# Performance work log

Measured on AMD Instinct MI355X. Metric: run time of the kernel, lower is better.

Reference implementation:

```python
import jax, jax.numpy as jnp
import numpy as np
import math

B, H, S, D = 2, 16, 2048, 64


def setup_inputs() -> dict:
    key = jax.random.key(0)
    kq, kk, kv = jax.random.split(key, 3)
    q = jax.random.normal(kq, (B, H, S, D), dtype=jnp.float32)
    k = jax.random.normal(kk, (B, H, S, D), dtype=jnp.float32)
    v = jax.random.normal(kv, (B, H, S, D), dtype=jnp.float32)
    # causal lower-triangular mask, broadcastable to [B, H, S, S]
    mask = jnp.tril(jnp.ones((S, S), dtype=jnp.int32))[None, None, :, :]
    return {"q": q, "k": k, "v": v, "mask": mask}


def reference(q, k, v, mask):
    d_tensor = q.shape[-1]
    # scores: [B, H, S, S] = q @ k^T / sqrt(d)
    scores = jnp.einsum("bhqd,bhkd->bhqk", q, k) / math.sqrt(d_tensor)
    scores = jnp.where(mask == 0, jnp.float32(-100000.0), scores)
    attn = jax.nn.softmax(scores, axis=-1)
    out = jnp.einsum("bhqk,bhkd->bhqd", attn, v)
    return (out, attn)
```

## Files before the change

kernel.cpp:

```cpp
#include <hip/hip_runtime.h>

#define S_LEN 2048
#define D_DIM 64
#define NBH   32
#define BQ    64
#define SCALE2 0.1803368801f
#define KST   72
#define PST   76

typedef _Float16 half8 __attribute__((ext_vector_type(8)));
typedef _Float16 half4 __attribute__((ext_vector_type(4)));
typedef float    fx4   __attribute__((ext_vector_type(4)));

__global__ __launch_bounds__(256, 3)
void attn_fused(const float* __restrict__ Q, const float* __restrict__ K,
                const float* __restrict__ V, float* __restrict__ Out,
                float* __restrict__ Attn) {
    const int bh  = blockIdx.x;
    const int qt  = (int)(gridDim.y - 1) - (int)blockIdx.y;
    const int q0  = qt * BQ;
    const int T   = qt + 1;

    const int tid  = threadIdx.x;
    const int lane = tid & 63;
    const int w    = tid >> 6;
    const int ln15 = lane & 15;
    const int quad = lane >> 4;

    __shared__ _Float16 q_s[BQ][KST];
    __shared__ _Float16 k_s[64][KST];
    __shared__ _Float16 v_t[64][KST];
    __shared__ _Float16 p_s[4][16][PST];

    const float* Qb = Q + ((size_t)bh * S_LEN + q0) * D_DIM;
    const float* Kb = K + (size_t)bh * S_LEN * D_DIM;
    const float* Vb = V + (size_t)bh * S_LEN * D_DIM;

    {
        const float4* src = (const float4*)Qb;
        #pragma unroll
        for (int u = 0; u < 4; ++u) {
            int i = u * 256 + tid;
            int r = i >> 4, c4 = i & 15;
            float4 f = src[i];
            half4 h = {(_Float16)(f.x * SCALE2), (_Float16)(f.y * SCALE2),
                       (_Float16)(f.z * SCALE2), (_Float16)(f.w * SCALE2)};
            *(half4*)&q_s[r][c4 * 4] = h;
        }
    }
    __syncthreads();

    const int mrow = w * 16 + ln15;
    const half8 a_q0 = *(const half8*)&q_s[mrow][quad * 8];
    const half8 a_q1 = *(const half8*)&q_s[mrow][32 + quad * 8];

    const int qrow0 = q0 + w * 16 + quad * 4;

    const int sr  = tid >> 4;
    const int sc4 = tid & 15;

    float l_r[4] = {0.f, 0.f, 0.f, 0.f};

    float4 kf0, kf1, kf2, kf3;
    {
        const float4* ks = (const float4*)Kb;
        kf0 = ks[tid]; kf1 = ks[256 + tid]; kf2 = ks[512 + tid]; kf3 = ks[768 + tid];
    }
    for (int t = 0; t < T; ++t) {
        {
            half4 h0 = {(_Float16)kf0.x, (_Float16)kf0.y, (_Float16)kf0.z, (_Float16)kf0.w};
            half4 h1 = {(_Float16)kf1.x, (_Float16)kf1.y, (_Float16)kf1.z, (_Float16)kf1.w};
            half4 h2 = {(_Float16)kf2.x, (_Float16)kf2.y, (_Float16)kf2.z, (_Float16)kf2.w};
            half4 h3 = {(_Float16)kf3.x, (_Float16)kf3.y, (_Float16)kf3.z, (_Float16)kf3.w};
            *(half4*)&k_s[sr +  0][sc4 * 4] = h0;
            *(half4*)&k_s[sr + 16][sc4 * 4] = h1;
            *(half4*)&k_s[sr + 32][sc4 * 4] = h2;
            *(half4*)&k_s[sr + 48][sc4 * 4] = h3;
        }
        __syncthreads();

        if (t + 1 < T) {
            const float4* kn = (const float4*)(Kb + (size_t)(t + 1) * 64 * D_DIM);
            kf0 = kn[tid]; kf1 = kn[256 + tid]; kf2 = kn[512 + tid]; kf3 = kn[768 + tid];
        }

        fx4 sC[4];
        #pragma unroll
        for (int nt = 0; nt < 4; ++nt) {
            fx4 z = {0.f, 0.f, 0.f, 0.f};
            half8 b0 = *(const half8*)&k_s[nt * 16 + ln15][quad * 8];
            half8 b1 = *(const half8*)&k_s[nt * 16 + ln15][32 + quad * 8];
            z = __builtin_amdgcn_mfma_f32_16x16x32_f16(a_q0, b0, z, 0, 0, 0);
            z = __builtin_amdgcn_mfma_f32_16x16x32_f16(a_q1, b1, z, 0, 0, 0);
            sC[nt] = z;
        }

        if (t < T - 1) {
            #pragma unroll
            for (int nt = 0; nt < 4; ++nt)
                #pragma unroll
                for (int r = 0; r < 4; ++r)
                    l_r[r] += exp2f(sC[nt][r]);
        } else {
            const int j0 = t * 64;
            #pragma unroll
            for (int nt = 0; nt < 4; ++nt) {
                int jc = j0 + nt * 16 + ln15;
                #pragma unroll
                for (int r = 0; r < 4; ++r) {
                    float x = (jc <= qrow0 + r) ? sC[nt][r] : -1e30f;
                    l_r[r] += exp2f(x);
                }
            }
        }
        __syncthreads();
    }

    float inv_l[4];
    #pragma unroll
    for (int r = 0; r < 4; ++r) {
        float s = l_r[r];
        s += __shfl_xor(s, 1);
        s += __shfl_xor(s, 2);
        s += __shfl_xor(s, 4);
        s += __shfl_xor(s, 8);
        inv_l[r] = 1.0f / s;
    }

    fx4 oacc[4];
    #pragma unroll
    for (int dt = 0; dt < 4; ++dt) oacc[dt] = (fx4){0.f, 0.f, 0.f, 0.f};

    const int vc4 = tid >> 4;
    const int vjg = tid & 15;

    float4 vf0, vf1, vf2, vf3;
    {
        const float4* ks = (const float4*)Kb;
        kf0 = ks[tid]; kf1 = ks[256 + tid]; kf2 = ks[512 + tid]; kf3 = ks[768 + tid];
        const float4* vs = (const float4*)Vb;
        vf0 = vs[(vjg * 4 + 0) * 16 + vc4];
        vf1 = vs[(vjg * 4 + 1) * 16 + vc4];
        vf2 = vs[(vjg * 4 + 2) * 16 + vc4];
        vf3 = vs[(vjg * 4 + 3) * 16 + vc4];
    }

    for (int t = 0; t < T; ++t) {
        const int j0 = t * 64;

        {
            half4 h0 = {(_Float16)kf0.x, (_Float16)kf0.y, (_Float16)kf0.z, (_Float16)kf0.w};
            half4 h1 = {(_Float16)kf1.x, (_Float16)kf1.y, (_Float16)kf1.z, (_Float16)kf1.w};
            half4 h2 = {(_Float16)kf2.x, (_Float16)kf2.y, (_Float16)kf2.z, (_Float16)kf2.w};
            half4 h3 = {(_Float16)kf3.x, (_Float16)kf3.y, (_Float16)kf3.z, (_Float16)kf3.w};
            *(half4*)&k_s[sr +  0][sc4 * 4] = h0;
            *(half4*)&k_s[sr + 16][sc4 * 4] = h1;
            *(half4*)&k_s[sr + 32][sc4 * 4] = h2;
            *(half4*)&k_s[sr + 48][sc4 * 4] = h3;
            half4 t0 = {(_Float16)vf0.x, (_Float16)vf1.x, (_Float16)vf2.x, (_Float16)vf3.x};
            half4 t1 = {(_Float16)vf0.y, (_Float16)vf1.y, (_Float16)vf2.y, (_Float16)vf3.y};
            half4 t2 = {(_Float16)vf0.z, (_Float16)vf1.z, (_Float16)vf2.z, (_Float16)vf3.z};
            half4 t3 = {(_Float16)vf0.w, (_Float16)vf1.w, (_Float16)vf2.w, (_Float16)vf3.w};
            *(half4*)&v_t[vc4 * 4 + 0][vjg * 4] = t0;
            *(half4*)&v_t[vc4 * 4 + 1][vjg * 4] = t1;
            *(half4*)&v_t[vc4 * 4 + 2][vjg * 4] = t2;
            *(half4*)&v_t[vc4 * 4 + 3][vjg * 4] = t3;
        }
        __syncthreads();

        if (t + 1 < T) {
            const float4* kn = (const float4*)(Kb + (size_t)(t + 1) * 64 * D_DIM);
            kf0 = kn[tid]; kf1 = kn[256 + tid]; kf2 = kn[512 + tid]; kf3 = kn[768 + tid];
            const float4* vn = (const float4*)(Vb + (size_t)(t + 1) * 64 * D_DIM);
            vf0 = vn[(vjg * 4 + 0) * 16 + vc4];
            vf1 = vn[(vjg * 4 + 1) * 16 + vc4];
            vf2 = vn[(vjg * 4 + 2) * 16 + vc4];
            vf3 = vn[(vjg * 4 + 3) * 16 + vc4];
        }

        fx4 sC[4];
        #pragma unroll
        for (int nt = 0; nt < 4; ++nt) {
            fx4 z = {0.f, 0.f, 0.f, 0.f};
            half8 b0 = *(const half8*)&k_s[nt * 16 + ln15][quad * 8];
            half8 b1 = *(const half8*)&k_s[nt * 16 + ln15][32 + quad * 8];
            z = __builtin_amdgcn_mfma_f32_16x16x32_f16(a_q0, b0, z, 0, 0, 0);
            z = __builtin_amdgcn_mfma_f32_16x16x32_f16(a_q1, b1, z, 0, 0, 0);
            sC[nt] = z;
        }

        if (t < T - 1) {
            #pragma unroll
            for (int nt = 0; nt < 4; ++nt) {
                int jc = j0 + nt * 16 + ln15;
                #pragma unroll
                for (int r = 0; r < 4; ++r) {
                    float p = exp2f(sC[nt][r]) * inv_l[r];
                    Attn[((size_t)bh * S_LEN + (size_t)(qrow0 + r)) * S_LEN + jc] = p;
                    p_s[w][quad * 4 + r][nt * 16 + ln15] = (_Float16)p;
                }
            }
        } else {
            #pragma unroll
            for (int nt = 0; nt < 4; ++nt) {
                int jc = j0 + nt * 16 + ln15;
                #pragma unroll
                for (int r = 0; r < 4; ++r) {
                    float x = (jc <= qrow0 + r) ? sC[nt][r] : -1e30f;
                    float p = exp2f(x) * inv_l[r];
                    Attn[((size_t)bh * S_LEN + (size_t)(qrow0 + r)) * S_LEN + jc] = p;
                    p_s[w][quad * 4 + r][nt * 16 + ln15] = (_Float16)p;
                }
            }
        }

        {
            half8 a_p0 = *(const half8*)&p_s[w][ln15][quad * 8];
            half8 a_p1 = *(const half8*)&p_s[w][ln15][32 + quad * 8];
            #pragma unroll
            for (int dt = 0; dt < 4; ++dt) {
                half8 bv0 = *(const half8*)&v_t[dt * 16 + ln15][quad * 8];
                half8 bv1 = *(const half8*)&v_t[dt * 16 + ln15][32 + quad * 8];
                oacc[dt] = __builtin_amdgcn_mfma_f32_16x16x32_f16(a_p0, bv0, oacc[dt], 0, 0, 0);
                oacc[dt] = __builtin_amdgcn_mfma_f32_16x16x32_f16(a_p1, bv1, oacc[dt], 0, 0, 0);
            }
        }
        __syncthreads();
    }

    #pragma unroll
    for (int dt = 0; dt < 4; ++dt) {
        #pragma unroll
        for (int r = 0; r < 4; ++r) {
            size_t oidx = ((size_t)bh * S_LEN + (size_t)(qrow0 + r)) * D_DIM + dt * 16 + ln15;
            Out[oidx] = oacc[dt][r];
        }
    }

    {
        const int jend = q0 + BQ;
        const int rowlen4 = (S_LEN - jend) >> 2;
        if (rowlen4 > 0) {
            fx4 z = {0.f, 0.f, 0.f, 0.f};
            for (int r = w; r < BQ; r += 4) {
                fx4* dst = (fx4*)(Attn + ((size_t)bh * S_LEN + (size_t)(q0 + r)) * S_LEN + jend);
                for (int c = lane; c < rowlen4; c += 64) dst[c] = z;
            }
        }
    }
}

extern "C" void kernel_launch(void* const* d_in, const int* in_sizes, int n_in,
                              void* d_out, int out_size, void* d_ws, size_t ws_size,
                              hipStream_t stream) {
    const float* q = (const float*)d_in[0];
    const float* k = (const float*)d_in[1];
    const float* v = (const float*)d_in[2];
    float* out  = (float*)d_out;
    float* attn = out + (size_t)NBH * S_LEN * D_DIM;
    dim3 grid(NBH, S_LEN / BQ);
    attn_fused<<<grid, 256, 0, stream>>>(q, k, v, out, attn);
}
```

Baseline: 683.3 us.

## Double-buffer K/V tiles in LDS and use lighter barriers

```diff
diff --git a/kernel.cpp b/kernel.cpp
--- a/kernel.cpp
+++ b/kernel.cpp
@@ -6,11 +6,16 @@
 #define BQ    64
 #define SCALE2 0.1803368801f
 #define KST   72
-#define PST   76
 
 typedef _Float16 half8 __attribute__((ext_vector_type(8)));
 typedef _Float16 half4 __attribute__((ext_vector_type(4)));
 typedef float    fx4   __attribute__((ext_vector_type(4)));
+
+#define BAR() do {                                            \
+    asm volatile("s_waitcnt lgkmcnt(0)" ::: "memory");        \
+    __builtin_amdgcn_s_barrier();                             \
+    asm volatile("" ::: "memory");                            \
+} while (0)
 
 __global__ __launch_bounds__(256, 3)
 void attn_fused(const float* __restrict__ Q, const float* __restrict__ K,
@@ -27,15 +32,25 @@
     const int ln15 = lane & 15;
     const int quad = lane >> 4;
 
-    __shared__ _Float16 q_s[BQ][KST];
-    __shared__ _Float16 k_s[64][KST];
-    __shared__ _Float16 v_t[64][KST];
-    __shared__ _Float16 p_s[4][16][PST];
+    __shared__ _Float16 smem[5 * 64 * KST];
+    _Float16 (*kb0)[KST] = (_Float16 (*)[KST])&smem[0];
+    _Float16 (*kb1)[KST] = (_Float16 (*)[KST])&smem[64 * KST];
+    _Float16 (*vb0)[KST] = (_Float16 (*)[KST])&smem[2 * 64 * KST];
+    _Float16 (*vb1)[KST] = (_Float16 (*)[KST])&smem[3 * 64 * KST];
+    _Float16 (*pw)[KST]  = (_Float16 (*)[KST])&smem[4 * 64 * KST + w * 16 * KST];
+    _Float16 (*q_s)[KST] = kb1;
 
     const float* Qb = Q + ((size_t)bh * S_LEN + q0) * D_DIM;
     const float* Kb = K + (size_t)bh * S_LEN * D_DIM;
     const float* Vb = V + (size_t)bh * S_LEN * D_DIM;
 
+    const int sr  = tid >> 4;
+    const int sc4 = tid & 15;
+    const int vc4 = tid >> 4;
+    const int vjg = tid & 15;
+
+    const float4* ks0 = (const float4*)Kb;
+    float4 kf0 = ks0[tid], kf1 = ks0[256 + tid], kf2 = ks0[512 + tid], kf3 = ks0[768 + tid];
     {
         const float4* src = (const float4*)Qb;
         #pragma unroll
@@ -56,28 +71,21 @@
 
     const int qrow0 = q0 + w * 16 + quad * 4;
 
-    const int sr  = tid >> 4;
-    const int sc4 = tid & 15;
-
     float l_r[4] = {0.f, 0.f, 0.f, 0.f};
 
-    float4 kf0, kf1, kf2, kf3;
-    {
-        const float4* ks = (const float4*)Kb;
-        kf0 = ks[tid]; kf1 = ks[256 + tid]; kf2 = ks[512 + tid]; kf3 = ks[768 + tid];
-    }
     for (int t = 0; t < T; ++t) {
+        _Float16 (*kb)[KST] = (t & 1) ? kb1 : kb0;
         {
             half4 h0 = {(_Float16)kf0.x, (_Float16)kf0.y, (_Float16)kf0.z, (_Float16)kf0.w};
             half4 h1 = {(_Float16)kf1.x, (_Float16)kf1.y, (_Float16)kf1.z, (_Float16)kf1.w};
             half4 h2 = {(_Float16)kf2.x, (_Float16)kf2.y, (_Float16)kf2.z, (_Float16)kf2.w};
             half4 h3 = {(_Float16)kf3.x, (_Float16)kf3.y, (_Float16)kf3.z, (_Float16)kf3.w};
-            *(half4*)&k_s[sr +  0][sc4 * 4] = h0;
-            *(half4*)&k_s[sr + 16][sc4 * 4] = h1;
-            *(half4*)&k_s[sr + 32][sc4 * 4] = h2;
-            *(half4*)&k_s[sr + 48][sc4 * 4] = h3;
-        }
-        __syncthreads();
+            *(half4*)&kb[sr +  0][sc4 * 4] = h0;
+            *(half4*)&kb[sr + 16][sc4 * 4] = h1;
+            *(half4*)&kb[sr + 32][sc4 * 4] = h2;
+            *(half4*)&kb[sr + 48][sc4 * 4] = h3;
+        }
+        BAR();
 
         if (t + 1 < T) {
             const float4* kn = (const float4*)(Kb + (size_t)(t + 1) * 64 * D_DIM);
@@ -88,8 +96,8 @@
         #pragma unroll
         for (int nt = 0; nt < 4; ++nt) {
             fx4 z = {0.f, 0.f, 0.f, 0.f};
-            half8 b0 = *(const half8*)&k_s[nt * 16 + ln15][quad * 8];
-            half8 b1 = *(const half8*)&k_s[nt * 16 + ln15][32 + quad * 8];
+            half8 b0 = *(const half8*)&kb[nt * 16 + ln15][quad * 8];
+            half8 b1 = *(const half8*)&kb[nt * 16 + ln15][32 + quad * 8];
             z = __builtin_amdgcn_mfma_f32_16x16x32_f16(a_q0, b0, z, 0, 0, 0);
             z = __builtin_amdgcn_mfma_f32_16x16x32_f16(a_q1, b1, z, 0, 0, 0);
             sC[nt] = z;
@@ -113,8 +121,8 @@
                 }
             }
         }
-        __syncthreads();
-    }
+    }
+    BAR();
 
     float inv_l[4];
     #pragma unroll
@@ -131,13 +139,9 @@
     #pragma unroll
     for (int dt = 0; dt < 4; ++dt) oacc[dt] = (fx4){0.f, 0.f, 0.f, 0.f};
 
-    const int vc4 = tid >> 4;
-    const int vjg = tid & 15;
-
     float4 vf0, vf1, vf2, vf3;
     {
-        const float4* ks = (const float4*)Kb;
-        kf0 = ks[tid]; kf1 = ks[256 + tid]; kf2 = ks[512 + tid]; kf3 = ks[768 + tid];
+        kf0 = ks0[tid]; kf1 = ks0[256 + tid]; kf2 = ks0[512 + tid]; kf3 = ks0[768 + tid];
         const float4* vs = (const float4*)Vb;
         vf0 = vs[(vjg * 4 + 0) * 16 + vc4];
         vf1 = vs[(vjg * 4 + 1) * 16 + vc4];
@@ -147,26 +151,28 @@
 
     for (int t = 0; t < T; ++t) {
         const int j0 = t * 64;
+        _Float16 (*kb)[KST] = (t & 1) ? kb1 : kb0;
+        _Float16 (*vb)[KST] = (t & 1) ? vb1 : vb0;
 
         {
             half4 h0 = {(_Float16)kf0.x, (_Float16)kf0.y, (_Float16)kf0.z, (_Float16)kf0.w};
             half4 h1 = {(_Float16)kf1.x, (_Float16)kf1.y, (_Float16)kf1.z, (_Float16)kf1.w};
             half4 h2 = {(_Float16)kf2.x, (_Float16)kf2.y, (_Float16)kf2.z, (_Float16)kf2.w};
             half4 h3 = {(_Float16)kf3.x, (_Float16)kf3.y, (_Float16)kf3.z, (_Float16)kf3.w};
-            *(half4*)&k_s[sr +  0][sc4 * 4] = h0;
-            *(half4*)&k_s[sr + 16][sc4 * 4] = h1;
-            *(half4*)&k_s[sr + 32][sc4 * 4] = h2;
-            *(half4*)&k_s[sr + 48][sc4 * 4] = h3;
+            *(half4*)&kb[sr +  0][sc4 * 4] = h0;
+            *(half4*)&kb[sr + 16][sc4 * 4] = h1;
+            *(half4*)&kb[sr + 32][sc4 * 4] = h2;
+            *(half4*)&kb[sr + 48][sc4 * 4] = h3;
             half4 t0 = {(_Float16)vf0.x, (_Float16)vf1.x, (_Float16)vf2.x, (_Float16)vf3.x};
             half4 t1 = {(_Float16)vf0.y, (_Float16)vf1.y, (_Float16)vf2.y, (_Float16)vf3.y};
             half4 t2 = {(_Float16)vf0.z, (_Float16)vf1.z, (_Float16)vf2.z, (_Float16)vf3.z};
             half4 t3 = {(_Float16)vf0.w, (_Float16)vf1.w, (_Float16)vf2.w, (_Float16)vf3.w};
-            *(half4*)&v_t[vc4 * 4 + 0][vjg * 4] = t0;
-            *(half4*)&v_t[vc4 * 4 + 1][vjg * 4] = t1;
-            *(half4*)&v_t[vc4 * 4 + 2][vjg * 4] = t2;
-            *(half4*)&v_t[vc4 * 4 + 3][vjg * 4] = t3;
-        }
-        __syncthreads();
+            *(half4*)&vb[vc4 * 4 + 0][vjg * 4] = t0;
+            *(half4*)&vb[vc4 * 4 + 1][vjg * 4] = t1;
+            *(half4*)&vb[vc4 * 4 + 2][vjg * 4] = t2;
+            *(half4*)&vb[vc4 * 4 + 3][vjg * 4] = t3;
+        }
+        BAR();
 
         if (t + 1 < T) {
             const float4* kn = (const float4*)(Kb + (size_t)(t + 1) * 64 * D_DIM);
@@ -182,8 +188,8 @@
         #pragma unroll
         for (int nt = 0; nt < 4; ++nt) {
             fx4 z = {0.f, 0.f, 0.f, 0.f};
-            half8 b0 = *(const half8*)&k_s[nt * 16 + ln15][quad * 8];
-            half8 b1 = *(const half8*)&k_s[nt * 16 + ln15][32 + quad * 8];
+            half8 b0 = *(const half8*)&kb[nt * 16 + ln15][quad * 8];
+            half8 b1 = *(const half8*)&kb[nt * 16 + ln15][32 + quad * 8];
             z = __builtin_amdgcn_mfma_f32_16x16x32_f16(a_q0, b0, z, 0, 0, 0);
             z = __builtin_amdgcn_mfma_f32_16x16x32_f16(a_q1, b1, z, 0, 0, 0);
             sC[nt] = z;
@@ -197,7 +203,7 @@
                 for (int r = 0; r < 4; ++r) {
                     float p = exp2f(sC[nt][r]) * inv_l[r];
                     Attn[((size_t)bh * S_LEN + (size_t)(qrow0 + r)) * S_LEN + jc] = p;
-                    p_s[w][quad * 4 + r][nt * 16 + ln15] = (_Float16)p;
+                    pw[quad * 4 + r][nt * 16 + ln15] = (_Float16)p;
                 }
             }
         } else {
@@ -209,23 +215,22 @@
                     float x = (jc <= qrow0 + r) ? sC[nt][r] : -1e30f;
                     float p = exp2f(x) * inv_l[r];
                     Attn[((size_t)bh * S_LEN + (size_t)(qrow0 + r)) * S_LEN + jc] = p;
-                    p_s[w][quad * 4 + r][nt * 16 + ln15] = (_Float16)p;
+                    pw[quad * 4 + r][nt * 16 + ln15] = (_Float16)p;
                 }
             }
         }
 
         {
-            half8 a_p0 = *(const half8*)&p_s[w][ln15][quad * 8];
-            half8 a_p1 = *(const half8*)&p_s[w][ln15][32 + quad * 8];
+            half8 a_p0 = *(const half8*)&pw[ln15][quad * 8];
+            half8 a_p1 = *(const half8*)&pw[ln15][32 + quad * 8];
             #pragma unroll
             for (int dt = 0; dt < 4; ++dt) {
-                half8 bv0 = *(const half8*)&v_t[dt * 16 + ln15][quad * 8];
-                half8 bv1 = *(const half8*)&v_t[dt * 16 + ln15][32 + quad * 8];
+                half8 bv0 = *(const half8*)&vb[dt * 16 + ln15][quad * 8];
+                half8 bv1 = *(const half8*)&vb[dt * 16 + ln15][32 + quad * 8];
                 oacc[dt] = __builtin_amdgcn_mfma_f32_16x16x32_f16(a_p0, bv0, oacc[dt], 0, 0, 0);
                 oacc[dt] = __builtin_amdgcn_mfma_f32_16x16x32_f16(a_p1, bv1, oacc[dt], 0, 0, 0);
             }
         }
-        __syncthreads();
     }
 
     #pragma unroll
```

After: 670.6 us. No clear change (-1.9%).
